# Performance work log

Hardware: AMD Instinct MI355X
Metric: run time of the kernel (lower is better)

Reference implementation:

```python
import jax, jax.numpy as jnp
import numpy as np
import math

M = 0.5
S = 64.0
EPS = 1e-12  # F.normalize eps


def _l2norm(v):
    n = jnp.sqrt(jnp.sum(v * v, axis=-1, keepdims=True))
    return v / jnp.maximum(n, EPS)


def setup_inputs() -> dict:
    key = jax.random.key(0)
    k1, k2, k3 = jax.random.split(key, 3)
    B, D, C = 1024, 512, 100000
    x = jax.random.normal(k1, (B, D), dtype=jnp.float32)
    weight = jax.random.normal(k2, (C, D), dtype=jnp.float32) * 0.01  # nn.init.normal_(std=0.01)
    target = jax.random.randint(k3, (B,), 0, C, dtype=jnp.int64)
    return {"x": x, "weight": weight, "target": target}


def reference(x, weight, target):
    # NormLinear with weight_norm=True, feature_norm=True -> cosine logits
    xn = _l2norm(x)                       # [B, D]
    wn = _l2norm(weight)                  # [C, D]
    cos = jnp.einsum('bd,cd->bc', xn, wn)  # [B, C]

    # _get_body (computed under no_grad in torch -> stop_gradient here)
    B = cos.shape[0]
    cos_t = jnp.take_along_axis(cos, target[:, None], axis=1)  # [B, 1]
    cond = cos_t > 0.0                    # easy_margin: clamp_min(cos_t,0).bool()
    new_zy = jnp.cos(jnp.arccos(jnp.clip(cos_t, -1.0, 1.0)) + M)
    new_zy = jnp.where(cond, new_zy, cos_t)  # easy_margin keep = cos_t
    diff = (new_zy - cos_t)[:, 0]         # [B]
    # one_hot * diff == scatter diff at (row, target) without dense one-hot
    body = jnp.zeros_like(cos).at[jnp.arange(B), target].add(diff)
    body = jax.lax.stop_gradient(body)

    return (cos + body) * S
```

## Files before the change

### kernel.cpp

```cpp
#include <hip/hip_runtime.h>
#include <hip/hip_bf16.h>
#include <math.h>

#define BDIM 1024
#define CDIM 100000
#define DDIM 512
#define LDS_STRIDE 72

typedef float f32x4 __attribute__((ext_vector_type(4)));
typedef short bf16x8 __attribute__((ext_vector_type(8)));

static __device__ __forceinline__ unsigned short f2bf(float f) {
    union { float f; unsigned int u; } v; v.f = f;
    unsigned int r = v.u + 0x7FFFu + ((v.u >> 16) & 1u);
    return (unsigned short)(r >> 16);
}

static __device__ __forceinline__ uint4 pack8(const float4 p, const float4 q) {
    union { unsigned short u[8]; uint4 v; } pk;
    pk.u[0] = f2bf(p.x); pk.u[1] = f2bf(p.y); pk.u[2] = f2bf(p.z); pk.u[3] = f2bf(p.w);
    pk.u[4] = f2bf(q.x); pk.u[5] = f2bf(q.y); pk.u[6] = f2bf(q.z); pk.u[7] = f2bf(q.w);
    return pk.v;
}

__global__ void xnorm_kernel(const float* __restrict__ x, unsigned short* __restrict__ xn) {
    const int row  = blockIdx.x * 4 + (threadIdx.x >> 6);
    const int lane = threadIdx.x & 63;
    const float* xr = x + row * DDIM;
    float4 a = *(const float4*)(xr + lane * 4);
    float4 b = *(const float4*)(xr + 256 + lane * 4);
    float s = a.x*a.x + a.y*a.y + a.z*a.z + a.w*a.w
            + b.x*b.x + b.y*b.y + b.z*b.z + b.w*b.w;
#pragma unroll
    for (int o = 32; o; o >>= 1) s += __shfl_xor(s, o);
    const float sc = 1.0f / fmaxf(sqrtf(s), 1e-12f);
    ushort4 o0, o1;
    o0.x = f2bf(a.x * sc); o0.y = f2bf(a.y * sc); o0.z = f2bf(a.z * sc); o0.w = f2bf(a.w * sc);
    o1.x = f2bf(b.x * sc); o1.y = f2bf(b.y * sc); o1.z = f2bf(b.z * sc); o1.w = f2bf(b.w * sc);
    *(ushort4*)(xn + row * DDIM + lane * 4)       = o0;
    *(ushort4*)(xn + row * DDIM + 256 + lane * 4) = o1;
}

__global__ void wnorm_kernel(const float* __restrict__ w, float* __restrict__ sw) {
    const int row  = blockIdx.x * 4 + (threadIdx.x >> 6);
    const int lane = threadIdx.x & 63;
    const float* wr = w + (size_t)row * DDIM;
    float4 a = *(const float4*)(wr + lane * 4);
    float4 b = *(const float4*)(wr + 256 + lane * 4);
    float s = a.x*a.x + a.y*a.y + a.z*a.z + a.w*a.w
            + b.x*b.x + b.y*b.y + b.z*b.z + b.w*b.w;
#pragma unroll
    for (int o = 32; o; o >>= 1) s += __shfl_xor(s, o);
    if (lane == 0) sw[row] = 1.0f / fmaxf(sqrtf(s), 1e-12f);
}

__global__ __launch_bounds__(256, 2)
void arc_gemm_kernel(const unsigned short* __restrict__ xn,
                     const float* __restrict__ w,
                     const float* __restrict__ sw,
                     const int* __restrict__ tgt,
                     float* __restrict__ out) {
    __shared__ unsigned short As[2][128 * LDS_STRIDE];
    __shared__ unsigned short Bs[2][128 * LDS_STRIDE];

    const int t    = threadIdx.x;
    const int lane = t & 63;
    const int wid  = t >> 6;
    const int mt   = blockIdx.x & 7;
    const int nt   = blockIdx.x >> 3;
    const int m0   = mt * 128;
    const int n0   = nt * 128;
    const int wm   = (wid & 1) * 64;
    const int wn   = (wid >> 1) * 64;

    const int sr = t >> 1;
    const int sk = (t & 1) * 32;

    const unsigned short* Ag = xn + (m0 + sr) * DDIM + sk;
    int brow = n0 + sr; brow = brow < CDIM ? brow : (CDIM - 1);
    const float* Bg = w + (size_t)brow * DDIM + sk;

    f32x4 acc[4][4] = {};
    uint4  ar[4];
    float4 br[8];

#define LOAD_TILE(kk) do {                                                     \
    _Pragma("unroll") for (int i = 0; i < 4; ++i)                              \
        ar[i] = *(const uint4*)(Ag + (kk) + i * 8);                            \
    _Pragma("unroll") for (int i = 0; i < 8; ++i)                              \
        br[i] = *(const float4*)(Bg + (kk) + i * 4);                           \
} while (0)

#define STORE_TILE(bufi) do {                                                  \
    unsigned short* ab = &As[bufi][sr * LDS_STRIDE + sk];                      \
    unsigned short* bb = &Bs[bufi][sr * LDS_STRIDE + sk];                      \
    _Pragma("unroll") for (int i = 0; i < 4; ++i)                              \
        *(uint4*)(ab + i * 8) = ar[i];                                         \
    _Pragma("unroll") for (int j = 0; j < 4; ++j)                              \
        *(uint4*)(bb + j * 8) = pack8(br[2 * j], br[2 * j + 1]);               \
} while (0)

#define MFMA_STEP(bufi) do {                                                   \
    _Pragma("unroll") for (int hk = 0; hk < 2; ++hk) {                         \
        bf16x8 av[4], bv[4];                                                   \
        const int ko = hk * 32 + (lane >> 4) * 8;                              \
        _Pragma("unroll") for (int f = 0; f < 4; ++f) {                        \
            av[f] = *(const bf16x8*)(&As[bufi][(wm + f * 16 + (lane & 15)) * LDS_STRIDE + ko]); \
            bv[f] = *(const bf16x8*)(&Bs[bufi][(wn + f * 16 + (lane & 15)) * LDS_STRIDE + ko]); \
        }                                                                      \
        _Pragma("unroll") for (int mf = 0; mf < 4; ++mf)                       \
            _Pragma("unroll") for (int nf = 0; nf < 4; ++nf)                   \
                acc[mf][nf] = __builtin_amdgcn_mfma_f32_16x16x32_bf16(         \
                    av[mf], bv[nf], acc[mf][nf], 0, 0, 0);                     \
    }                                                                          \
} while (0)

    LOAD_TILE(0);
    STORE_TILE(0);
#pragma unroll
    for (int ks = 0; ks < 8; ++ks) {
        const int cur = ks & 1;
        if (ks < 7) LOAD_TILE((ks + 1) * 64);
        __syncthreads();
        MFMA_STEP(cur);
        if (ks < 7) STORE_TILE(cur ^ 1);
    }

    float swv[4];
    int   gcv[4];
#pragma unroll
    for (int nf = 0; nf < 4; ++nf) {
        int gc = n0 + wn + nf * 16 + (lane & 15);
        gcv[nf] = gc;
        swv[nf] = sw[gc < CDIM ? gc : (CDIM - 1)];
    }
#pragma unroll
    for (int mf = 0; mf < 4; ++mf) {
#pragma unroll
        for (int j = 0; j < 4; ++j) {
            const int grow = m0 + wm + mf * 16 + (lane >> 4) * 4 + j;
            const int tg = tgt[grow];
            float* orow = out + (size_t)grow * CDIM;
#pragma unroll
            for (int nf = 0; nf < 4; ++nf) {
                const int gc = gcv[nf];
                if (gc < CDIM) {
                    float v = acc[mf][nf][j] * swv[nf];
                    if (gc == tg) {
                        float cv = fminf(fmaxf(v, -1.0f), 1.0f);
                        if (v > 0.0f)
                            v = cv * 0.87758256189037276f
                              - sqrtf(fmaxf(0.0f, 1.0f - cv * cv)) * 0.47942553860420301f;
                    }
                    orow[gc] = v * 64.0f;
                }
            }
        }
    }
#undef LOAD_TILE
#undef STORE_TILE
#undef MFMA_STEP
}

extern "C" void kernel_launch(void* const* d_in, const int* in_sizes, int n_in,
                              void* d_out, int out_size, void* d_ws, size_t ws_size,
                              hipStream_t stream) {
    const float* x   = (const float*)d_in[0];
    const float* w   = (const float*)d_in[1];
    const int*   tgt = (const int*)d_in[2];
    float* out = (float*)d_out;

    unsigned short* xn = (unsigned short*)d_ws;
    float* sw = (float*)((char*)d_ws + (size_t)BDIM * DDIM * 2);

    hipLaunchKernelGGL(xnorm_kernel, dim3(BDIM / 4), dim3(256), 0, stream, x, xn);
    hipLaunchKernelGGL(wnorm_kernel, dim3(CDIM / 4), dim3(256), 0, stream, w, sw);

    const int ntiles = (CDIM + 127) / 128;
    hipLaunchKernelGGL(arc_gemm_kernel, dim3(8 * ntiles), dim3(256), 0, stream,
                       xn, w, sw, tgt, out);
}
```

Baseline: 618.6 us.

## Pre-normalize weights to bf16 and compute target margin in fp64

The weight normalization pass now writes a bf16 normalized copy of W to workspace, so the GEMM reads half the bytes and skips in-loop fp32-to-bf16 packing and per-column scaling. A separate kernel computes the exact target cosine in double precision and the margin difference, which the epilogue just adds. The fast GEMM uses a single LDS buffer, requests three blocks per CU, and remaps block indices to group column tiles. The cost is an extra full write and read of the 100MB-scale bf16 weight copy plus one extra small kernel. The old path is kept as a fallback when workspace is too small.

```diff
diff --git a/kernel.cpp b/kernel.cpp
--- a/kernel.cpp
+++ b/kernel.cpp
@@ -5,7 +5,8 @@
 #define BDIM 1024
 #define CDIM 100000
 #define DDIM 512
-#define LDS_STRIDE 72
+#define FB_STRIDE 72
+#define FS 72
 
 typedef float f32x4 __attribute__((ext_vector_type(4)));
 typedef short bf16x8 __attribute__((ext_vector_type(8)));
@@ -23,12 +24,13 @@
     return pk.v;
 }
 
-__global__ void xnorm_kernel(const float* __restrict__ x, unsigned short* __restrict__ xn) {
+__global__ void rownorm_bf16_kernel(const float* __restrict__ in,
+                                    unsigned short* __restrict__ outp) {
     const int row  = blockIdx.x * 4 + (threadIdx.x >> 6);
     const int lane = threadIdx.x & 63;
-    const float* xr = x + row * DDIM;
-    float4 a = *(const float4*)(xr + lane * 4);
-    float4 b = *(const float4*)(xr + 256 + lane * 4);
+    const float* r = in + (size_t)row * DDIM;
+    float4 a = *(const float4*)(r + lane * 4);
+    float4 b = *(const float4*)(r + 256 + lane * 4);
     float s = a.x*a.x + a.y*a.y + a.z*a.z + a.w*a.w
             + b.x*b.x + b.y*b.y + b.z*b.z + b.w*b.w;
 #pragma unroll
@@ -37,8 +39,8 @@
     ushort4 o0, o1;
     o0.x = f2bf(a.x * sc); o0.y = f2bf(a.y * sc); o0.z = f2bf(a.z * sc); o0.w = f2bf(a.w * sc);
     o1.x = f2bf(b.x * sc); o1.y = f2bf(b.y * sc); o1.z = f2bf(b.z * sc); o1.w = f2bf(b.w * sc);
-    *(ushort4*)(xn + row * DDIM + lane * 4)       = o0;
-    *(ushort4*)(xn + row * DDIM + 256 + lane * 4) = o1;
+    *(ushort4*)(outp + (size_t)row * DDIM + lane * 4)       = o0;
+    *(ushort4*)(outp + (size_t)row * DDIM + 256 + lane * 4) = o1;
 }
 
 __global__ void wnorm_kernel(const float* __restrict__ w, float* __restrict__ sw) {
@@ -54,14 +56,150 @@
     if (lane == 0) sw[row] = 1.0f / fmaxf(sqrtf(s), 1e-12f);
 }
 
+__global__ void tdiff_kernel(const float* __restrict__ x,
+                             const float* __restrict__ w,
+                             const int* __restrict__ tgt,
+                             float* __restrict__ diff) {
+    const int row  = blockIdx.x * 4 + (threadIdx.x >> 6);
+    const int lane = threadIdx.x & 63;
+    const int tg   = tgt[row];
+    const float* xr = x + (size_t)row * DDIM;
+    const float* wr = w + (size_t)tg * DDIM;
+    double xx = 0.0, ww = 0.0, xw = 0.0;
+#pragma unroll
+    for (int i = 0; i < 2; ++i) {
+        float4 a = *(const float4*)(xr + i * 256 + lane * 4);
+        float4 b = *(const float4*)(wr + i * 256 + lane * 4);
+        xx += (double)a.x*a.x + (double)a.y*a.y + (double)a.z*a.z + (double)a.w*a.w;
+        ww += (double)b.x*b.x + (double)b.y*b.y + (double)b.z*b.z + (double)b.w*b.w;
+        xw += (double)a.x*b.x + (double)a.y*b.y + (double)a.z*b.z + (double)a.w*b.w;
+    }
+#pragma unroll
+    for (int o = 32; o; o >>= 1) {
+        xx += __shfl_xor(xx, o);
+        ww += __shfl_xor(ww, o);
+        xw += __shfl_xor(xw, o);
+    }
+    if (lane == 0) {
+        float nx = fmaxf((float)sqrt(xx), 1e-12f);
+        float nw = fmaxf((float)sqrt(ww), 1e-12f);
+        float cos_t = (float)xw / (nx * nw);
+        float d = 0.0f;
+        if (cos_t > 0.0f) {
+            float cv = fminf(fmaxf(cos_t, -1.0f), 1.0f);
+            d = cv * 0.87758256189037276f
+              - sqrtf(fmaxf(0.0f, 1.0f - cv * cv)) * 0.47942553860420301f
+              - cos_t;
+        }
+        diff[row] = d;
+    }
+}
+
+__global__ __launch_bounds__(256, 3)
+void arc_gemm_fast(const unsigned short* __restrict__ xn,
+                   const unsigned short* __restrict__ wn,
+                   const int* __restrict__ tgt,
+                   const float* __restrict__ diff,
+                   float* __restrict__ out) {
+    __shared__ unsigned short As[128 * FS];
+    __shared__ unsigned short Bs[128 * FS];
+
+    const int t    = threadIdx.x;
+    const int lane = t & 63;
+    const int wid  = t >> 6;
+
+    const int logical = (blockIdx.x & 7) * 782 + (blockIdx.x >> 3);
+    const int mt = logical & 7;
+    const int nt = logical >> 3;
+    const int m0 = mt * 128;
+    const int n0 = nt * 128;
+    const int wm = (wid & 1) * 64;
+    const int wnc = (wid >> 1) * 64;
+
+    const int sr = t >> 1;
+    const int sk = (t & 1) * 32;
+    const unsigned short* Ag = xn + (size_t)(m0 + sr) * DDIM + sk;
+    int brow = n0 + sr; brow = brow < CDIM ? brow : (CDIM - 1);
+    const unsigned short* Bg = wn + (size_t)brow * DDIM + sk;
+    unsigned short* al = &As[sr * FS + sk];
+    unsigned short* bl = &Bs[sr * FS + sk];
+
+    f32x4 acc[4][4] = {};
+    uint4 ar[4], br[4];
+
+#pragma unroll
+    for (int i = 0; i < 4; ++i) {
+        ar[i] = *(const uint4*)(Ag + i * 8);
+        br[i] = *(const uint4*)(Bg + i * 8);
+    }
+
+#pragma unroll
+    for (int ks = 0; ks < 8; ++ks) {
+#pragma unroll
+        for (int i = 0; i < 4; ++i) {
+            *(uint4*)(al + i * 8) = ar[i];
+            *(uint4*)(bl + i * 8) = br[i];
+        }
+        __syncthreads();
+        if (ks < 7) {
+#pragma unroll
+            for (int i = 0; i < 4; ++i) {
+                ar[i] = *(const uint4*)(Ag + (ks + 1) * 64 + i * 8);
+                br[i] = *(const uint4*)(Bg + (ks + 1) * 64 + i * 8);
+            }
+        }
+#pragma unroll
+        for (int hk = 0; hk < 2; ++hk) {
+            bf16x8 av[4], bv[4];
+            const int ko = hk * 32 + (lane >> 4) * 8;
+#pragma unroll
+            for (int f = 0; f < 4; ++f) {
+                av[f] = *(const bf16x8*)(&As[(wm  + f * 16 + (lane & 15)) * FS + ko]);
+                bv[f] = *(const bf16x8*)(&Bs[(wnc + f * 16 + (lane & 15)) * FS + ko]);
+            }
+#pragma unroll
+            for (int mf = 0; mf < 4; ++mf)
+#pragma unroll
+                for (int nf = 0; nf < 4; ++nf)
+                    acc[mf][nf] = __builtin_amdgcn_mfma_f32_16x16x32_bf16(
+                        av[mf], bv[nf], acc[mf][nf], 0, 0, 0);
+        }
+        if (ks < 7) __syncthreads();
+    }
+
+    int gcv[4];
+#pragma unroll
+    for (int nf = 0; nf < 4; ++nf) gcv[nf] = n0 + wnc + nf * 16 + (lane & 15);
+#pragma unroll
+    for (int mf = 0; mf < 4; ++mf) {
+#pragma unroll
+        for (int j = 0; j < 4; ++j) {
+            const int grow = m0 + wm + mf * 16 + (lane >> 4) * 4 + j;
+            const int tg = tgt[grow];
+            const float dv = diff[grow];
+            float* orow = out + (size_t)grow * CDIM;
+#pragma unroll
+            for (int nf = 0; nf < 4; ++nf) {
+                const int gc = gcv[nf];
+                if (gc < CDIM) {
+                    float v = acc[mf][nf][j];
+                    if (gc == tg) v += dv;
+                    orow[gc] = v * 64.0f;
+                }
+            }
+        }
+    }
+}
+
 __global__ __launch_bounds__(256, 2)
 void arc_gemm_kernel(const unsigned short* __restrict__ xn,
                      const float* __restrict__ w,
                      const float* __restrict__ sw,
                      const int* __restrict__ tgt,
+                     const float* __restrict__ diff,
                      float* __restrict__ out) {
-    __shared__ unsigned short As[2][128 * LDS_STRIDE];
-    __shared__ unsigned short Bs[2][128 * LDS_STRIDE];
+    __shared__ unsigned short As[2][128 * FB_STRIDE];
+    __shared__ unsigned short Bs[2][128 * FB_STRIDE];
 
     const int t    = threadIdx.x;
     const int lane = t & 63;
@@ -92,8 +230,8 @@
 } while (0)
 
 #define STORE_TILE(bufi) do {                                                  \
-    unsigned short* ab = &As[bufi][sr * LDS_STRIDE + sk];                      \
-    unsigned short* bb = &Bs[bufi][sr * LDS_STRIDE + sk];                      \
+    unsigned short* ab = &As[bufi][sr * FB_STRIDE + sk];                       \
+    unsigned short* bb = &Bs[bufi][sr * FB_STRIDE + sk];                       \
     _Pragma("unroll") for (int i = 0; i < 4; ++i)                              \
         *(uint4*)(ab + i * 8) = ar[i];                                         \
     _Pragma("unroll") for (int j = 0; j < 4; ++j)                              \
@@ -105,8 +243,8 @@
         bf16x8 av[4], bv[4];                                                   \
         const int ko = hk * 32 + (lane >> 4) * 8;                              \
         _Pragma("unroll") for (int f = 0; f < 4; ++f) {                        \
-            av[f] = *(const bf16x8*)(&As[bufi][(wm + f * 16 + (lane & 15)) * LDS_STRIDE + ko]); \
-            bv[f] = *(const bf16x8*)(&Bs[bufi][(wn + f * 16 + (lane & 15)) * LDS_STRIDE + ko]); \
+            av[f] = *(const bf16x8*)(&As[bufi][(wm + f * 16 + (lane & 15)) * FB_STRIDE + ko]); \
+            bv[f] = *(const bf16x8*)(&Bs[bufi][(wn + f * 16 + (lane & 15)) * FB_STRIDE + ko]); \
         }                                                                      \
         _Pragma("unroll") for (int mf = 0; mf < 4; ++mf)                       \
             _Pragma("unroll") for (int nf = 0; nf < 4; ++nf)                   \
@@ -140,18 +278,14 @@
         for (int j = 0; j < 4; ++j) {
             const int grow = m0 + wm + mf * 16 + (lane >> 4) * 4 + j;
             const int tg = tgt[grow];
+            const float dv = diff[grow];
             float* orow = out + (size_t)grow * CDIM;
 #pragma unroll
             for (int nf = 0; nf < 4; ++nf) {
                 const int gc = gcv[nf];
                 if (gc < CDIM) {
                     float v = acc[mf][nf][j] * swv[nf];
-                    if (gc == tg) {
-                        float cv = fminf(fmaxf(v, -1.0f), 1.0f);
-                        if (v > 0.0f)
-                            v = cv * 0.87758256189037276f
-                              - sqrtf(fmaxf(0.0f, 1.0f - cv * cv)) * 0.47942553860420301f;
-                    }
+                    if (gc == tg) v += dv;
                     orow[gc] = v * 64.0f;
                 }
             }
@@ -171,12 +305,24 @@
     float* out = (float*)d_out;
 
     unsigned short* xn = (unsigned short*)d_ws;
-    float* sw = (float*)((char*)d_ws + (size_t)BDIM * DDIM * 2);
-
-    hipLaunchKernelGGL(xnorm_kernel, dim3(BDIM / 4), dim3(256), 0, stream, x, xn);
-    hipLaunchKernelGGL(wnorm_kernel, dim3(CDIM / 4), dim3(256), 0, stream, w, sw);
-
+    const size_t xn_bytes   = (size_t)BDIM * DDIM * 2;
+    float* diff = (float*)((char*)d_ws + xn_bytes);
+    const size_t diff_bytes = (size_t)BDIM * 4;
+    const size_t wn_bytes   = (size_t)CDIM * DDIM * 2;
     const int ntiles = (CDIM + 127) / 128;
-    hipLaunchKernelGGL(arc_gemm_kernel, dim3(8 * ntiles), dim3(256), 0, stream,
-                       xn, w, sw, tgt, out);
-}
+
+    hipLaunchKernelGGL(rownorm_bf16_kernel, dim3(BDIM / 4), dim3(256), 0, stream, x, xn);
+    hipLaunchKernelGGL(tdiff_kernel, dim3(BDIM / 4), dim3(256), 0, stream, x, w, tgt, diff);
+
+    if (ws_size >= xn_bytes + diff_bytes + wn_bytes) {
+        unsigned short* wnb = (unsigned short*)((char*)d_ws + xn_bytes + diff_bytes);
+        hipLaunchKernelGGL(rownorm_bf16_kernel, dim3(CDIM / 4), dim3(256), 0, stream, w, wnb);
+        hipLaunchKernelGGL(arc_gemm_fast, dim3(8 * ntiles), dim3(256), 0, stream,
+                           xn, wnb, tgt, diff, out);
+    } else {
+        float* sw = (float*)((char*)d_ws + xn_bytes + diff_bytes);
+        hipLaunchKernelGGL(wnorm_kernel, dim3(CDIM / 4), dim3(256), 0, stream, w, sw);
+        hipLaunchKernelGGL(arc_gemm_kernel, dim3(8 * ntiles), dim3(256), 0, stream,
+                           xn, w, sw, tgt, diff, out);
+    }
+}
```

Result: slower. 826.5 us (+33.6%).
